# Performance work log

Hardware: AMD Instinct MI355X
Metric: run time of the kernel (lower is better)

The kernel has to match this reference:

```python
import jax, jax.numpy as jnp
import numpy as np

N_EMBD = 1024
N_HEAD = 16


def setup_inputs() -> dict:
    key = jax.random.key(0)
    ks = jax.random.split(key, 5)
    C = N_EMBD
    x = jax.random.normal(ks[0], (4, 2048, C), dtype=jnp.float32)
    s = 1.0 / np.sqrt(C)
    W_attn = jax.random.normal(ks[1], (C, 3 * C), dtype=jnp.float32) * s
    b_attn = jnp.zeros((3 * C,), dtype=jnp.float32)
    W_proj = jax.random.normal(ks[2], (C, C), dtype=jnp.float32) * s
    b_proj = jnp.zeros((C,), dtype=jnp.float32)
    return {"x": x, "W_attn": W_attn, "b_attn": b_attn, "W_proj": W_proj, "b_proj": b_proj}


def reference(x, W_attn, b_attn, W_proj, b_proj):
    B, T, C = x.shape
    H = N_HEAD
    D = C // H
    qkv = x @ W_attn + b_attn                      # [B,T,3C]
    q, k, v = jnp.split(qkv, 3, axis=-1)
    # [B,H,T,D]
    q = q.reshape(B, T, H, D).transpose(0, 2, 1, 3)
    k = k.reshape(B, T, H, D).transpose(0, 2, 1, 3)
    v = v.reshape(B, T, H, D).transpose(0, 2, 1, 3)
    scale = 1.0 / jnp.sqrt(jnp.asarray(D, dtype=x.dtype))
    att = jnp.einsum('bhqd,bhkd->bhqk', q, k) * scale   # [B,H,T,T]
    causal = jnp.tril(jnp.ones((T, T), dtype=bool))
    att = jnp.where(causal, att, jnp.finfo(att.dtype).min)
    att = jax.nn.softmax(att, axis=-1)
    y = jnp.einsum('bhqk,bhkd->bhqd', att, v)            # [B,H,T,D]
    y = y.transpose(0, 2, 1, 3).reshape(B, T, C)
    return y @ W_proj + b_proj
```

## Files before the change

### kernel.cpp

```cpp
#include <hip/hip_runtime.h>
#include <type_traits>

typedef __attribute__((ext_vector_type(8))) short short8;
typedef __attribute__((ext_vector_type(8))) unsigned short ushort8;
typedef __attribute__((ext_vector_type(4))) float floatx4;
typedef __attribute__((ext_vector_type(2))) unsigned int uintx2v;

__device__ __forceinline__ unsigned short f2bf(float f) {
    union { float f; unsigned int i; } v;
    v.f = f;
    unsigned int u = v.i;
    unsigned int r = (u + 0x7FFFu + ((u >> 16) & 1u)) >> 16;
    return (unsigned short)r;
}

__device__ __forceinline__ void gload_lds16(const unsigned short* g, unsigned short* lds_base) {
    __builtin_amdgcn_global_load_lds(
        (const __attribute__((address_space(1))) unsigned int*)g,
        (__attribute__((address_space(3))) unsigned int*)lds_base,
        16, 0, 0);
}

__device__ __forceinline__ void pbar() {
    asm volatile("" ::: "memory");
    __builtin_amdgcn_s_barrier();
    asm volatile("" ::: "memory");
}

__global__ __launch_bounds__(256) void cvt_f32_bf16_kernel(
    const float* __restrict__ src, unsigned short* __restrict__ dst, int n8)
{
    int i = blockIdx.x * 256 + threadIdx.x;
    if (i >= n8) return;
    const float4* s = (const float4*)src + (size_t)i * 2;
    float4 a = s[0];
    float4 b = s[1];
    ushort8 r;
    r[0] = f2bf(a.x); r[1] = f2bf(a.y); r[2] = f2bf(a.z); r[3] = f2bf(a.w);
    r[4] = f2bf(b.x); r[5] = f2bf(b.y); r[6] = f2bf(b.z); r[7] = f2bf(b.w);
    *((ushort8*)dst + i) = r;
}

__global__ __launch_bounds__(256) void transpose_cvt_kernel(
    const float* __restrict__ src, unsigned short* __restrict__ dst, int K, int N)
{
    __shared__ float tile[32][33];
    const int tx = threadIdx.x & 31;
    const int ty = threadIdx.x >> 5;
    const int k0 = blockIdx.y * 32, n0 = blockIdx.x * 32;
#pragma unroll
    for (int i = 0; i < 4; ++i)
        tile[ty + i * 8][tx] = src[(size_t)(k0 + ty + i * 8) * N + n0 + tx];
    __syncthreads();
#pragma unroll
    for (int i = 0; i < 4; ++i)
        dst[(size_t)(n0 + ty + i * 8) * K + k0 + tx] = f2bf(tile[tx][ty + i * 8]);
}

template <int MODE, typename OutT>
__global__ __launch_bounds__(256) void gemm128_kernel(
    const unsigned short* __restrict__ A,
    const unsigned short* __restrict__ Bt,
    const float* __restrict__ bias,
    OutT* __restrict__ C,
    unsigned short* __restrict__ Qo,
    unsigned short* __restrict__ Ko,
    unsigned short* __restrict__ Vto,
    int M, int N, int K)
{
    __shared__ __align__(16) unsigned short As[2][128 * 32];
    __shared__ __align__(16) unsigned short Bs[2][128 * 32];

    const int tid  = threadIdx.x;
    const int lane = tid & 63;
    const int w    = tid >> 6;
    const int wm   = w & 1;
    const int wn   = w >> 1;
    const int quad = lane >> 4;
    const int l16  = lane & 15;

    const int m0 = blockIdx.y * 128;
    const int n0 = blockIdx.x * 128;

    floatx4 acc[4][4];
#pragma unroll
    for (int i = 0; i < 4; ++i)
#pragma unroll
        for (int j = 0; j < 4; ++j) acc[i][j] = (floatx4)0.0f;

    const int r0 = tid >> 2;
    const int kc = (((tid & 3) ^ ((tid >> 3) & 3)) << 3);
    const unsigned short* Ag = A  + (size_t)(m0 + r0) * K + kc;
    const unsigned short* Bg = Bt + (size_t)(n0 + r0) * K + kc;

    const int sw = ((quad ^ ((l16 >> 1) & 3)) << 3);

    const int nt = K >> 5;

#define STAGE(buf, t)                                                          \
    do {                                                                       \
        const int kk = (t) << 5;                                               \
        gload_lds16(Ag + kk,                    &As[buf][w * 512]);            \
        gload_lds16(Ag + (size_t)64 * K + kk,   &As[buf][w * 512 + 2048]);     \
        gload_lds16(Bg + kk,                    &Bs[buf][w * 512]);            \
        gload_lds16(Bg + (size_t)64 * K + kk,   &Bs[buf][w * 512 + 2048]);     \
    } while (0)

    STAGE(0, 0);

    for (int t = 0; t < nt; ++t) {
        const int b = t & 1;
        if (t + 1 < nt) {
            STAGE(b ^ 1, t + 1);
            asm volatile("s_waitcnt vmcnt(4)" ::: "memory");
        } else {
            asm volatile("s_waitcnt vmcnt(0)" ::: "memory");
        }
        pbar();

        short8 a[4], bb[4];
#pragma unroll
        for (int mi = 0; mi < 4; ++mi)
            a[mi] = *(const short8*)&As[b][(wm * 64 + mi * 16 + l16) * 32 + sw];
#pragma unroll
        for (int ni = 0; ni < 4; ++ni)
            bb[ni] = *(const short8*)&Bs[b][(wn * 64 + ni * 16 + l16) * 32 + sw];
#pragma unroll
        for (int mi = 0; mi < 4; ++mi)
#pragma unroll
            for (int ni = 0; ni < 4; ++ni)
                acc[mi][ni] = __builtin_amdgcn_mfma_f32_16x16x32_bf16(a[mi], bb[ni], acc[mi][ni], 0, 0, 0);
        pbar();
    }
#undef STAGE

#pragma unroll
    for (int ni = 0; ni < 4; ++ni) {
        const int n = n0 + wn * 64 + ni * 16 + l16;
        const float bval = bias[n];
        const int seg = n >> 10;
        const int nl  = n & 1023;
#pragma unroll
        for (int mi = 0; mi < 4; ++mi) {
            if constexpr (MODE == 0) {
#pragma unroll
                for (int r = 0; r < 4; ++r) {
                    const int m = m0 + wm * 64 + mi * 16 + (quad << 2) + r;
                    const float val = acc[mi][ni][r] + bval;
                    if constexpr (std::is_same<OutT, unsigned short>::value)
                        C[(size_t)m * N + n] = f2bf(val);
                    else
                        C[(size_t)m * N + n] = val;
                }
            } else {
                if (seg < 2) {
                    unsigned short* P = (seg == 0) ? Qo : Ko;
#pragma unroll
                    for (int r = 0; r < 4; ++r) {
                        const int m = m0 + wm * 64 + mi * 16 + (quad << 2) + r;
                        P[(size_t)m * 1024 + nl] = f2bf(acc[mi][ni][r] + bval);
                    }
                } else {
                    const int mb = m0 + wm * 64 + mi * 16 + (quad << 2);
                    const int bbk = mb >> 11, t0 = mb & 2047;
                    unsigned int lo = (unsigned int)f2bf(acc[mi][ni][0] + bval) |
                                      ((unsigned int)f2bf(acc[mi][ni][1] + bval) << 16);
                    unsigned int hi = (unsigned int)f2bf(acc[mi][ni][2] + bval) |
                                      ((unsigned int)f2bf(acc[mi][ni][3] + bval) << 16);
                    uint2 pv; pv.x = lo; pv.y = hi;
                    *(uint2*)(Vto + ((size_t)bbk * 1024 + nl) * 2048 + t0) = pv;
                }
            }
        }
    }
}

__device__ __forceinline__ void softmax_pack(
    const floatx4* s, bool masked, int key0, int qg, int kq4,
    float& l_run, short8& pf0o, short8& pf1o)
{
    const float SC2 = 0.18033688011112042f;
    const float MB2 = -17.312340490667562f;
    unsigned int plo[4], phi[4];
    if (!masked) {
#pragma unroll
        for (int ks = 0; ks < 4; ++ks) {
            float pv0 = __builtin_amdgcn_exp2f(fmaf(s[ks][0], SC2, MB2));
            float pv1 = __builtin_amdgcn_exp2f(fmaf(s[ks][1], SC2, MB2));
            float pv2 = __builtin_amdgcn_exp2f(fmaf(s[ks][2], SC2, MB2));
            float pv3 = __builtin_amdgcn_exp2f(fmaf(s[ks][3], SC2, MB2));
            l_run += (pv0 + pv1) + (pv2 + pv3);
            asm("v_cvt_pk_bf16_f32 %0, %1, %2" : "=v"(plo[ks]) : "v"(pv0), "v"(pv1));
            asm("v_cvt_pk_bf16_f32 %0, %1, %2" : "=v"(phi[ks]) : "v"(pv2), "v"(pv3));
        }
    } else {
#pragma unroll
        for (int ks = 0; ks < 4; ++ks) {
            const int kb = key0 + (ks << 4) + kq4;
            float a0 = (kb + 0 <= qg) ? fmaf(s[ks][0], SC2, MB2) : -100000.0f;
            float a1 = (kb + 1 <= qg) ? fmaf(s[ks][1], SC2, MB2) : -100000.0f;
            float a2 = (kb + 2 <= qg) ? fmaf(s[ks][2], SC2, MB2) : -100000.0f;
            float a3 = (kb + 3 <= qg) ? fmaf(s[ks][3], SC2, MB2) : -100000.0f;
            float pv0 = __builtin_amdgcn_exp2f(a0);
            float pv1 = __builtin_amdgcn_exp2f(a1);
            float pv2 = __builtin_amdgcn_exp2f(a2);
            float pv3 = __builtin_amdgcn_exp2f(a3);
            l_run += (pv0 + pv1) + (pv2 + pv3);
            asm("v_cvt_pk_bf16_f32 %0, %1, %2" : "=v"(plo[ks]) : "v"(pv0), "v"(pv1));
            asm("v_cvt_pk_bf16_f32 %0, %1, %2" : "=v"(phi[ks]) : "v"(pv2), "v"(pv3));
        }
    }
    uintx2v t0 = __builtin_amdgcn_permlane32_swap(plo[0], plo[1], false, false);
    uintx2v u0 = __builtin_amdgcn_permlane16_swap(t0[0], t0[1], false, false);
    uintx2v t1 = __builtin_amdgcn_permlane32_swap(phi[0], phi[1], false, false);
    uintx2v u1 = __builtin_amdgcn_permlane16_swap(t1[0], t1[1], false, false);
    uintx2v t2 = __builtin_amdgcn_permlane32_swap(plo[2], plo[3], false, false);
    uintx2v u2 = __builtin_amdgcn_permlane16_swap(t2[0], t2[1], false, false);
    uintx2v t3 = __builtin_amdgcn_permlane32_swap(phi[2], phi[3], false, false);
    uintx2v u3 = __builtin_amdgcn_permlane16_swap(t3[0], t3[1], false, false);
    union { unsigned int d[4]; short8 v; } fa, fb;
    fa.d[0] = u0[0]; fa.d[1] = u1[0]; fa.d[2] = u0[1]; fa.d[3] = u1[1];
    fb.d[0] = u2[0]; fb.d[1] = u3[0]; fb.d[2] = u2[1]; fb.d[3] = u3[1];
    pf0o = fa.v;
    pf1o = fb.v;
}

__global__ __launch_bounds__(256, 4) void attn_kernel(
    const unsigned short* __restrict__ Q,
    const unsigned short* __restrict__ Kq,
    const unsigned short* __restrict__ Vt,
    unsigned short* __restrict__ Y)
{
    const int T = 2048;

    int idx = blockIdx.x;
    int g   = idx >> 6;
    int qtp = (g & 4) ? ((g & 8) ? (g - 8) : (g - 4))
                      : ((g & 8) ? (19 - g) : (15 - g));
    int bh  = idx & 63;
    int b   = bh >> 4;
    int h   = bh & 15;

    const int tid  = threadIdx.x;
    const int lane = tid & 63;
    const int w    = tid >> 6;
    const int quad = lane >> 4;
    const int l16  = lane & 15;

    __shared__ __align__(16) unsigned short Ks2[8 * 64 * 8];
    __shared__ __align__(16) unsigned short Vs2[8 * 64 * 8];

    const int qb = qtp * 128 + (w << 5);

    const unsigned short* qpa = Q + (size_t)(b * T + qb + l16) * 1024 + h * 64;
    const unsigned short* qpb = qpa + (size_t)16 * 1024;
    short8 qfa0 = *(const short8*)(qpa + (quad << 3));
    short8 qfa1 = *(const short8*)(qpa + 32 + (quad << 3));
    short8 qfb0 = *(const short8*)(qpb + (quad << 3));
    short8 qfb1 = *(const short8*)(qpb + 32 + (quad << 3));

    float lra = 0.0f, lrb = 0.0f;
    floatx4 oa[4], ob[4];
#pragma unroll
    for (int ns = 0; ns < 4; ++ns) { oa[ns] = (floatx4)0.0f; ob[ns] = (floatx4)0.0f; }

    const unsigned short* kg0p = Kq + (size_t)(b * T + lane) * 1024 + h * 64 + (w) * 8;
    const unsigned short* kg1p = Kq + (size_t)(b * T + lane) * 1024 + h * 64 + (w + 4) * 8;
    const unsigned short* vg0p = Vt + ((size_t)(b * 1024 + h * 64 + lane)) * 2048 + (w) * 8;
    const unsigned short* vg1p = Vt + ((size_t)(b * 1024 + h * 64 + lane)) * 2048 + (w + 4) * 8;

    const int qa_g = qb + l16;
    const int qb_g = qb + 16 + l16;
    const int kq4  = quad << 2;

    const int ktiles = 2 * qtp + 2;
    for (int kt = 0; kt < ktiles; ++kt) {
        const int key0 = kt << 6;
        __syncthreads();
        gload_lds16(kg0p + (size_t)key0 * 1024, Ks2 + (w) * 512);
        gload_lds16(kg1p + (size_t)key0 * 1024, Ks2 + (w + 4) * 512);
        gload_lds16(vg0p + key0, Vs2 + (w) * 512);
        gload_lds16(vg1p + key0, Vs2 + (w + 4) * 512);
        __syncthreads();

        if (key0 <= qb + 31) {
            floatx4 sa[4], sb[4];
#pragma unroll
            for (int ks = 0; ks < 4; ++ks) {
                short8 kf0 = *(const short8*)&Ks2[((0 * 4 + quad) * 64 + ks * 16 + l16) * 8];
                short8 kf1 = *(const short8*)&Ks2[((1 * 4 + quad) * 64 + ks * 16 + l16) * 8];
                sa[ks] = __builtin_amdgcn_mfma_f32_16x16x32_bf16(kf0, qfa0, (floatx4)0.0f, 0, 0, 0);
                sa[ks] = __builtin_amdgcn_mfma_f32_16x16x32_bf16(kf1, qfa1, sa[ks], 0, 0, 0);
                sb[ks] = __builtin_amdgcn_mfma_f32_16x16x32_bf16(kf0, qfb0, (floatx4)0.0f, 0, 0, 0);
                sb[ks] = __builtin_amdgcn_mfma_f32_16x16x32_bf16(kf1, qfb1, sb[ks], 0, 0, 0);
            }

            const bool masked = (key0 + 64 > qb);
            short8 pa0, pa1, pb0, pb1;
            softmax_pack(sa, masked, key0, qa_g, kq4, lra, pa0, pa1);
            softmax_pack(sb, masked, key0, qb_g, kq4, lrb, pb0, pb1);

#pragma unroll
            for (int ns = 0; ns < 4; ++ns) {
                short8 vf0 = *(const short8*)&Vs2[((0 * 4 + quad) * 64 + ns * 16 + l16) * 8];
                short8 vf1 = *(const short8*)&Vs2[((1 * 4 + quad) * 64 + ns * 16 + l16) * 8];
                oa[ns] = __builtin_amdgcn_mfma_f32_16x16x32_bf16(pa0, vf0, oa[ns], 0, 0, 0);
                oa[ns] = __builtin_amdgcn_mfma_f32_16x16x32_bf16(pa1, vf1, oa[ns], 0, 0, 0);
                ob[ns] = __builtin_amdgcn_mfma_f32_16x16x32_bf16(pb0, vf0, ob[ns], 0, 0, 0);
                ob[ns] = __builtin_amdgcn_mfma_f32_16x16x32_bf16(pb1, vf1, ob[ns], 0, 0, 0);
            }
        }
    }

    float sa_ = lra;
    sa_ += __shfl_xor(sa_, 16, 64);
    sa_ += __shfl_xor(sa_, 32, 64);
    const float lia = 1.0f / sa_;
    float sb_ = lrb;
    sb_ += __shfl_xor(sb_, 16, 64);
    sb_ += __shfl_xor(sb_, 32, 64);
    const float lib = 1.0f / sb_;

    float la[4], lb[4];
#pragma unroll
    for (int r = 0; r < 4; ++r) {
        la[r] = __shfl(lia, (quad << 2) + r, 64);
        lb[r] = __shfl(lib, (quad << 2) + r, 64);
    }

#pragma unroll
    for (int ns = 0; ns < 4; ++ns) {
        int d = (ns << 4) + l16;
#pragma unroll
        for (int r = 0; r < 4; ++r) {
            int ta = qb + (quad << 2) + r;
            Y[(size_t)(b * T + ta) * 1024 + h * 64 + d]        = f2bf(oa[ns][r] * la[r]);
            Y[(size_t)(b * T + ta + 16) * 1024 + h * 64 + d]   = f2bf(ob[ns][r] * lb[r]);
        }
    }
}

extern "C" void kernel_launch(void* const* d_in, const int* in_sizes, int n_in,
                              void* d_out, int out_size, void* d_ws, size_t ws_size,
                              hipStream_t stream) {
    const float* x  = (const float*)d_in[0];
    const float* Wa = (const float*)d_in[1];
    const float* ba = (const float*)d_in[2];
    const float* Wp = (const float*)d_in[3];
    const float* bp = (const float*)d_in[4];
    float* out = (float*)d_out;

    const size_t NX = (size_t)8192 * 1024;

    unsigned short* Qb  = (unsigned short*)d_ws;
    unsigned short* Kb  = Qb  + NX;
    unsigned short* Vtb = Kb  + NX;
    unsigned short* Yb  = Vtb + NX;
    unsigned short* xb  = Yb  + NX;
    unsigned short* Wat = xb  + NX;
    unsigned short* Wpt = Wat + (size_t)3072 * 1024;

    cvt_f32_bf16_kernel<<<(int)(NX / 8 / 256), 256, 0, stream>>>(x, xb, (int)(NX / 8));
    transpose_cvt_kernel<<<dim3(3072 / 32, 1024 / 32), 256, 0, stream>>>(Wa, Wat, 1024, 3072);
    transpose_cvt_kernel<<<dim3(1024 / 32, 1024 / 32), 256, 0, stream>>>(Wp, Wpt, 1024, 1024);

    gemm128_kernel<1, unsigned short><<<dim3(3072 / 128, 8192 / 128), 256, 0, stream>>>(
        xb, Wat, ba, (unsigned short*)nullptr, Qb, Kb, Vtb, 8192, 3072, 1024);

    attn_kernel<<<4 * 16 * (2048 / 128), 256, 0, stream>>>(Qb, Kb, Vtb, Yb);

    gemm128_kernel<0, float><<<dim3(1024 / 128, 8192 / 128), 256, 0, stream>>>(
        Yb, Wpt, bp, out, nullptr, nullptr, nullptr, 8192, 1024, 1024);
}
```

Before: 246.3 us.

## Enlarge GEMM tiles to 256x256x64 with 8 waves and interleaved staging

Replaces the 128x128 GEMM with a 256x256 tile, K-step 64 and 512 threads. Each wave now computes 128x64, and LDS fragment loads and global-to-LDS staging are interleaved between MFMA groups, using s_setprio around the MFMA bursts. The aim is better operand reuse and less global traffic per FLOP. In exchange, the output-projection GEMM launches only 128 blocks, fewer than the number of CUs, and the larger LDS footprint limits occupancy.

```diff
diff --git a/kernel.cpp b/kernel.cpp
--- a/kernel.cpp
+++ b/kernel.cpp
@@ -58,7 +58,7 @@
 }
 
 template <int MODE, typename OutT>
-__global__ __launch_bounds__(256) void gemm128_kernel(
+__global__ __launch_bounds__(512, 2) void gemm256_kernel(
     const unsigned short* __restrict__ A,
     const unsigned short* __restrict__ Bt,
     const float* __restrict__ bias,
@@ -68,71 +68,141 @@
     unsigned short* __restrict__ Vto,
     int M, int N, int K)
 {
-    __shared__ __align__(16) unsigned short As[2][128 * 32];
-    __shared__ __align__(16) unsigned short Bs[2][128 * 32];
+    __shared__ __align__(16) unsigned short As[2][256 * 64];
+    __shared__ __align__(16) unsigned short Bs[2][256 * 64];
 
     const int tid  = threadIdx.x;
     const int lane = tid & 63;
     const int w    = tid >> 6;
-    const int wm   = w & 1;
-    const int wn   = w >> 1;
+    const int wm   = w >> 2;
+    const int wn   = w & 3;
     const int quad = lane >> 4;
     const int l16  = lane & 15;
 
-    const int m0 = blockIdx.y * 128;
-    const int n0 = blockIdx.x * 128;
-
-    floatx4 acc[4][4];
-#pragma unroll
-    for (int i = 0; i < 4; ++i)
+    const int m0 = blockIdx.y * 256;
+    const int n0 = blockIdx.x * 256;
+
+    floatx4 acc[8][4];
+#pragma unroll
+    for (int i = 0; i < 8; ++i)
 #pragma unroll
         for (int j = 0; j < 4; ++j) acc[i][j] = (floatx4)0.0f;
 
-    const int r0 = tid >> 2;
-    const int kc = (((tid & 3) ^ ((tid >> 3) & 3)) << 3);
-    const unsigned short* Ag = A  + (size_t)(m0 + r0) * K + kc;
-    const unsigned short* Bg = Bt + (size_t)(n0 + r0) * K + kc;
-
-    const int sw = ((quad ^ ((l16 >> 1) & 3)) << 3);
-
-    const int nt = K >> 5;
-
-#define STAGE(buf, t)                                                          \
-    do {                                                                       \
-        const int kk = (t) << 5;                                               \
-        gload_lds16(Ag + kk,                    &As[buf][w * 512]);            \
-        gload_lds16(Ag + (size_t)64 * K + kk,   &As[buf][w * 512 + 2048]);     \
-        gload_lds16(Bg + kk,                    &Bs[buf][w * 512]);            \
-        gload_lds16(Bg + (size_t)64 * K + kk,   &Bs[buf][w * 512 + 2048]);     \
-    } while (0)
-
-    STAGE(0, 0);
+    const int srow = tid >> 3;
+    const int skc  = (((tid & 7) ^ ((tid >> 3) & 7)) << 3);
+    const unsigned short* Ag = A  + (size_t)(m0 + srow) * K + skc;
+    const unsigned short* Bg = Bt + (size_t)(n0 + srow) * K + skc;
+
+    const int swz = l16 & 7;
+
+    const int nt = K >> 6;
+
+#define STA(buf, t, i) gload_lds16(Ag + (size_t)((i) * 64) * K + (t) * 64, &As[buf][(i) * 4096 + w * 512])
+#define STB(buf, t, i) gload_lds16(Bg + (size_t)((i) * 64) * K + (t) * 64, &Bs[buf][(i) * 4096 + w * 512])
+#define ASLOT(ks) ((((ks) * 4 + quad) ^ swz) << 3)
+
+#pragma unroll
+    for (int i = 0; i < 4; ++i) STA(0, 0, i);
+#pragma unroll
+    for (int i = 0; i < 4; ++i) STB(0, 0, i);
+    asm volatile("s_waitcnt vmcnt(0)" ::: "memory");
+    pbar();
 
     for (int t = 0; t < nt; ++t) {
         const int b = t & 1;
+        const unsigned short* Ab = &As[b][0];
+        const unsigned short* Bb = &Bs[b][0];
+
+        short8 bfr[4][2], af[2][2];
+#pragma unroll
+        for (int ni = 0; ni < 4; ++ni)
+#pragma unroll
+            for (int ks = 0; ks < 2; ++ks)
+                bfr[ni][ks] = *(const short8*)&Bb[(wn * 64 + ni * 16 + l16) * 64 + ASLOT(ks)];
+#pragma unroll
+        for (int x = 0; x < 2; ++x)
+#pragma unroll
+            for (int ks = 0; ks < 2; ++ks)
+                af[x][ks] = *(const short8*)&Ab[(wm * 128 + x * 16 + l16) * 64 + ASLOT(ks)];
         if (t + 1 < nt) {
-            STAGE(b ^ 1, t + 1);
-            asm volatile("s_waitcnt vmcnt(4)" ::: "memory");
-        } else {
-            asm volatile("s_waitcnt vmcnt(0)" ::: "memory");
-        }
-        pbar();
-
-        short8 a[4], bb[4];
-#pragma unroll
-        for (int mi = 0; mi < 4; ++mi)
-            a[mi] = *(const short8*)&As[b][(wm * 64 + mi * 16 + l16) * 32 + sw];
-#pragma unroll
-        for (int ni = 0; ni < 4; ++ni)
-            bb[ni] = *(const short8*)&Bs[b][(wn * 64 + ni * 16 + l16) * 32 + sw];
-#pragma unroll
-        for (int mi = 0; mi < 4; ++mi)
+#pragma unroll
+            for (int i = 0; i < 4; ++i) STA(b ^ 1, t + 1, i);
+        }
+        pbar();
+        asm volatile("s_waitcnt lgkmcnt(0)" ::: "memory");
+        __builtin_amdgcn_s_setprio(1);
+#pragma unroll
+        for (int x = 0; x < 2; ++x)
 #pragma unroll
             for (int ni = 0; ni < 4; ++ni)
-                acc[mi][ni] = __builtin_amdgcn_mfma_f32_16x16x32_bf16(a[mi], bb[ni], acc[mi][ni], 0, 0, 0);
-        pbar();
-    }
-#undef STAGE
+#pragma unroll
+                for (int ks = 0; ks < 2; ++ks)
+                    acc[x][ni] = __builtin_amdgcn_mfma_f32_16x16x32_bf16(af[x][ks], bfr[ni][ks], acc[x][ni], 0, 0, 0);
+        __builtin_amdgcn_s_setprio(0);
+        pbar();
+
+#pragma unroll
+        for (int x = 0; x < 2; ++x)
+#pragma unroll
+            for (int ks = 0; ks < 2; ++ks)
+                af[x][ks] = *(const short8*)&Ab[(wm * 128 + (2 + x) * 16 + l16) * 64 + ASLOT(ks)];
+        if (t + 1 < nt) {
+#pragma unroll
+            for (int i = 0; i < 4; ++i) STB(b ^ 1, t + 1, i);
+        }
+        pbar();
+        asm volatile("s_waitcnt lgkmcnt(0)" ::: "memory");
+        __builtin_amdgcn_s_setprio(1);
+#pragma unroll
+        for (int x = 0; x < 2; ++x)
+#pragma unroll
+            for (int ni = 0; ni < 4; ++ni)
+#pragma unroll
+                for (int ks = 0; ks < 2; ++ks)
+                    acc[2 + x][ni] = __builtin_amdgcn_mfma_f32_16x16x32_bf16(af[x][ks], bfr[ni][ks], acc[2 + x][ni], 0, 0, 0);
+        __builtin_amdgcn_s_setprio(0);
+        pbar();
+
+#pragma unroll
+        for (int x = 0; x < 2; ++x)
+#pragma unroll
+            for (int ks = 0; ks < 2; ++ks)
+                af[x][ks] = *(const short8*)&Ab[(wm * 128 + (4 + x) * 16 + l16) * 64 + ASLOT(ks)];
+        pbar();
+        asm volatile("s_waitcnt lgkmcnt(0)" ::: "memory");
+        __builtin_amdgcn_s_setprio(1);
+#pragma unroll
+        for (int x = 0; x < 2; ++x)
+#pragma unroll
+            for (int ni = 0; ni < 4; ++ni)
+#pragma unroll
+                for (int ks = 0; ks < 2; ++ks)
+                    acc[4 + x][ni] = __builtin_amdgcn_mfma_f32_16x16x32_bf16(af[x][ks], bfr[ni][ks], acc[4 + x][ni], 0, 0, 0);
+        __builtin_amdgcn_s_setprio(0);
+        pbar();
+
+#pragma unroll
+        for (int x = 0; x < 2; ++x)
+#pragma unroll
+            for (int ks = 0; ks < 2; ++ks)
+                af[x][ks] = *(const short8*)&Ab[(wm * 128 + (6 + x) * 16 + l16) * 64 + ASLOT(ks)];
+        pbar();
+        asm volatile("s_waitcnt lgkmcnt(0)" ::: "memory");
+        __builtin_amdgcn_s_setprio(1);
+#pragma unroll
+        for (int x = 0; x < 2; ++x)
+#pragma unroll
+            for (int ni = 0; ni < 4; ++ni)
+#pragma unroll
+                for (int ks = 0; ks < 2; ++ks)
+                    acc[6 + x][ni] = __builtin_amdgcn_mfma_f32_16x16x32_bf16(af[x][ks], bfr[ni][ks], acc[6 + x][ni], 0, 0, 0);
+        __builtin_amdgcn_s_setprio(0);
+        asm volatile("s_waitcnt vmcnt(0)" ::: "memory");
+        pbar();
+    }
+#undef STA
+#undef STB
+#undef ASLOT
 
 #pragma unroll
     for (int ni = 0; ni < 4; ++ni) {
@@ -141,11 +211,11 @@
         const int seg = n >> 10;
         const int nl  = n & 1023;
 #pragma unroll
-        for (int mi = 0; mi < 4; ++mi) {
+        for (int mi = 0; mi < 8; ++mi) {
             if constexpr (MODE == 0) {
 #pragma unroll
                 for (int r = 0; r < 4; ++r) {
-                    const int m = m0 + wm * 64 + mi * 16 + (quad << 2) + r;
+                    const int m = m0 + wm * 128 + mi * 16 + (quad << 2) + r;
                     const float val = acc[mi][ni][r] + bval;
                     if constexpr (std::is_same<OutT, unsigned short>::value)
                         C[(size_t)m * N + n] = f2bf(val);
@@ -157,11 +227,11 @@
                     unsigned short* P = (seg == 0) ? Qo : Ko;
 #pragma unroll
                     for (int r = 0; r < 4; ++r) {
-                        const int m = m0 + wm * 64 + mi * 16 + (quad << 2) + r;
+                        const int m = m0 + wm * 128 + mi * 16 + (quad << 2) + r;
                         P[(size_t)m * 1024 + nl] = f2bf(acc[mi][ni][r] + bval);
                     }
                 } else {
-                    const int mb = m0 + wm * 64 + mi * 16 + (quad << 2);
+                    const int mb = m0 + wm * 128 + mi * 16 + (quad << 2);
                     const int bbk = mb >> 11, t0 = mb & 2047;
                     unsigned int lo = (unsigned int)f2bf(acc[mi][ni][0] + bval) |
                                       ((unsigned int)f2bf(acc[mi][ni][1] + bval) << 16);
@@ -364,11 +434,11 @@
     transpose_cvt_kernel<<<dim3(3072 / 32, 1024 / 32), 256, 0, stream>>>(Wa, Wat, 1024, 3072);
     transpose_cvt_kernel<<<dim3(1024 / 32, 1024 / 32), 256, 0, stream>>>(Wp, Wpt, 1024, 1024);
 
-    gemm128_kernel<1, unsigned short><<<dim3(3072 / 128, 8192 / 128), 256, 0, stream>>>(
+    gemm256_kernel<1, unsigned short><<<dim3(3072 / 256, 8192 / 256), 512, 0, stream>>>(
         xb, Wat, ba, (unsigned short*)nullptr, Qb, Kb, Vtb, 8192, 3072, 1024);
 
     attn_kernel<<<4 * 16 * (2048 / 128), 256, 0, stream>>>(Qb, Kb, Vtb, Yb);
 
-    gemm128_kernel<0, float><<<dim3(1024 / 128, 8192 / 128), 256, 0, stream>>>(
+    gemm256_kernel<0, float><<<dim3(1024 / 256, 8192 / 256), 512, 0, stream>>>(
         Yb, Wpt, bp, out, nullptr, nullptr, nullptr, 8192, 1024, 1024);
 }
```

Measured after the change: 268.3 us. +8.9%, slower.
